# Optimization experiments

Measured on AMD Instinct MI355X. Metric: run time of the kernel, lower is better.

The kernel has to match this reference:

```python
import jax, jax.numpy as jnp
import numpy as np

N = 8192        # nodes in batch
E = 262144      # edges (avg degree 32)
IN_C = 64
OUT_C = 64
K = 3           # max_k
G = 64          # graphs in batch
NC = 10         # n_class
EPS = 1e-5      # batchnorm eps


def setup_inputs() -> dict:
    key = jax.random.key(0)
    ks = jax.random.split(key, 16)
    D_in = IN_C * K    # 192
    D_out = OUT_C * K  # 192
    inp = {
        'x': jax.random.normal(ks[0], (N, IN_C), jnp.float32),
        'edge_index': jax.random.randint(ks[1], (2, E), 0, N, dtype=jnp.int64),
        'batch': jnp.sort(jax.random.randint(ks[2], (N,), 0, G, dtype=jnp.int64)),
        # spectral-normed masked linear
        'W_orig': jax.random.normal(ks[3], (D_out, D_in), jnp.float32) * 0.05,
        'b': jnp.zeros((D_out,), jnp.float32),
        'u': jax.random.normal(ks[4], (D_out,), jnp.float32),
        # batchnorms (training-mode batch stats)
        'bn1_gamma': jnp.ones((D_out,), jnp.float32),
        'bn1_beta': jnp.zeros((D_out,), jnp.float32),
        'bn2_gamma': jnp.ones((D_out * 3,), jnp.float32),
        'bn2_beta': jnp.zeros((D_out * 3,), jnp.float32),
        # funnel head
        'w1': jax.random.normal(ks[5], (D_out * 2, D_out * 3), jnp.float32) * 0.05,
        'b1': jnp.zeros((D_out * 2,), jnp.float32),
        'w2': jax.random.normal(ks[6], (D_out, D_out * 2), jnp.float32) * 0.05,
        'b2': jnp.zeros((D_out,), jnp.float32),
        'w3': jax.random.normal(ks[7], (NC, D_out), jnp.float32) * 0.05,
        'b3': jnp.zeros((NC,), jnp.float32),
    }
    return inp


def _forward(x, edge_index, batch, W_orig, b, u, bn1_gamma, bn1_beta,
             bn2_gamma, bn2_beta, w1, b1, w2, b2, w3, b3):
    n = x.shape[0]
    row, col = edge_index[0], edge_index[1]
    # sym-normalized Laplacian L = I - D^-1/2 A D^-1/2, densified ([N,N])
    deg = jnp.zeros((n,), x.dtype).at[row].add(1.0)
    dinv = jnp.where(deg > 0, jax.lax.rsqrt(jnp.maximum(deg, 1.0)), 0.0)
    vals = -dinv[row] * dinv[col]
    L = jnp.zeros((n, n), x.dtype).at[row, col].add(vals)
    idx = jnp.arange(n)
    L = L.at[idx, idx].add(1.0)
    Hs = [x]
    h = x
    for _ in range(K - 1):
        h = L @ h
        Hs.append(h)
    Hcat = jnp.concatenate(Hs, axis=1)              # [N, IN_C*K]
    # spectral norm of W (one power-iteration step with stored u)
    v = W_orig.T @ u
    v = v / (jnp.linalg.norm(v) + 1e-12)
    sigma = u @ (W_orig @ v)
    W = W_orig / sigma
    # block lower-triangular mask: block i passes first IN_C*(i+1) input cols
    col_idx = jnp.arange(IN_C * K)
    row_block = jnp.arange(OUT_C * K) // OUT_C
    mask = (col_idx[None, :] < IN_C * (row_block[:, None] + 1)).astype(W.dtype)
    H = Hcat @ (W * mask).T + b                     # masked linear
    # reservoir_act_fun is identity (default)
    mu, var = H.mean(0), H.var(0)                   # BN (batch stats)
    H = bn1_gamma * (H - mu) * jax.lax.rsqrt(var + EPS) + bn1_beta
    # fused-style triple pooling over graph ids
    Hsum = jax.ops.segment_sum(H, batch, num_segments=G)
    cnt = jax.ops.segment_sum(jnp.ones((n,), H.dtype), batch, num_segments=G)
    Havg = Hsum / jnp.maximum(cnt, 1.0)[:, None]
    Hmax = jax.ops.segment_max(H, batch, num_segments=G)
    Hg = jnp.concatenate([Havg, Hsum, Hmax], axis=1)  # [G, 3*OUT_C*K]
    mu2, var2 = Hg.mean(0), Hg.var(0)
    xo = bn2_gamma * (Hg - mu2) * jax.lax.rsqrt(var2 + EPS) + bn2_beta
    # funnel output (dropout = identity in eval)
    xo = jax.nn.relu(xo @ w1.T + b1)
    xo = jax.nn.relu(xo @ w2.T + b2)
    return jax.nn.log_softmax(xo @ w3.T + b3, axis=1)


def reference(x, edge_index, batch, W_orig, b, u, bn1_gamma, bn1_beta,
              bn2_gamma, bn2_beta, w1, b1, w2, b2, w3, b3):
    return _forward(x, edge_index, batch, W_orig, b, u, bn1_gamma, bn1_beta,
                    bn2_gamma, bn2_beta, w1, b1, w2, b2, w3, b3)
```

## Files before the change

### kernel.cpp

```cpp
#include <hip/hip_runtime.h>
#include <math.h>

#define NN   8192
#define EE   262144
#define CIN  64
#define DD   192
#define GG   64
#define NCLS 10
#define D3   576
#define F1   384
#define F2   192
#define EPSB 1e-5f
#define NB   64
#define EPB  (EE / NB)
#define PS   8

__global__ __launch_bounds__(1024) void count_kernel(const int* __restrict__ ei,
                                                     int* __restrict__ pcnt) {
    __shared__ int hist[NN];
    int b = blockIdx.x, t = threadIdx.x;
    int4* hz = (int4*)hist;
    for (int i = t; i < NN / 4; i += 1024) hz[i] = make_int4(0, 0, 0, 0);
    __syncthreads();
    int e0 = b * EPB;
    for (int i = t; i < EPB; i += 1024) atomicAdd(&hist[ei[e0 + i]], 1);
    __syncthreads();
    const int4* hs = (const int4*)hist;
    int4* p4 = (int4*)&pcnt[b * NN];
    for (int i = t; i < NN / 4; i += 1024) p4[i] = hs[i];
}

__global__ __launch_bounds__(256) void offs_kernel(int* __restrict__ pcnt,
                                                   int* __restrict__ deg,
                                                   float* __restrict__ dinv) {
    int i = blockIdx.x * 256 + threadIdx.x;
    int run = 0;
#pragma unroll
    for (int b = 0; b < NB; b++) {
        int v = pcnt[b * NN + i];
        pcnt[b * NN + i] = run;
        run += v;
    }
    deg[i] = run;
    dinv[i] = (run > 0) ? rsqrtf((float)run) : 0.f;
}

__global__ void scan_kernel(const int* __restrict__ deg, int* __restrict__ rowptr,
                            const int* __restrict__ batch, int* __restrict__ gstart) {
    __shared__ int part[256];
    int t = threadIdx.x;
    int local[32];
    int base = t * 32;
    int s = 0;
    for (int i = 0; i < 32; i++) { local[i] = s; s += deg[base + i]; }
    part[t] = s;
    __syncthreads();
    for (int off = 1; off < 256; off <<= 1) {
        int v = (t >= off) ? part[t - off] : 0;
        __syncthreads();
        part[t] += v;
        __syncthreads();
    }
    int prefix = (t > 0) ? part[t - 1] : 0;
    for (int i = 0; i < 32; i++) rowptr[base + i] = prefix + local[i];
    if (t == 255) rowptr[NN] = part[255];
    for (int i = t; i < NN; i += 256) {
        int b0 = batch[i];
        int b1 = (i + 1 < NN) ? batch[i + 1] : GG;
        if (i == 0) { for (int g = 0; g <= b0; g++) gstart[g] = 0; }
        for (int g = b0 + 1; g <= b1; g++) gstart[g] = i + 1;
    }
}

__global__ __launch_bounds__(1024) void scatter_kernel(const int* __restrict__ ei,
                                                       const int* __restrict__ rowptr,
                                                       const int* __restrict__ off,
                                                       unsigned short* __restrict__ csr_col) {
    __shared__ int cur[NN];
    int b = blockIdx.x, t = threadIdx.x;
    const int* ob = &off[b * NN];
    for (int i = t; i < NN; i += 1024) cur[i] = rowptr[i] + ob[i];
    __syncthreads();
    int e0 = b * EPB;
    for (int i = t; i < EPB; i += 1024) {
        int r = ei[e0 + i];
        int c = ei[EE + e0 + i];
        int pos = atomicAdd(&cur[r], 1);
        csr_col[pos] = (unsigned short)c;
    }
}

__global__ __launch_bounds__(256) void spmm_kernel(const float* __restrict__ hin,
    int in_stride, int in_off,
    const int* __restrict__ rowptr, const unsigned short* __restrict__ col,
    const float* __restrict__ dinv,
    float* __restrict__ Hcat, int coff, int write_self) {
    int idx = blockIdx.x * 256 + threadIdx.x;
    int row = idx >> 6;
    int lane = idx & 63;
    int s = rowptr[row], e = rowptr[row + 1];
    float acc0 = 0.f, acc1 = 0.f;
    int p = s;
    for (; p + 1 < e; p += 2) {
        int c0 = col[p], c1 = col[p + 1];
        acc0 += dinv[c0] * hin[c0 * in_stride + in_off + lane];
        acc1 += dinv[c1] * hin[c1 * in_stride + in_off + lane];
    }
    if (p < e) {
        int c = col[p];
        acc0 += dinv[c] * hin[c * in_stride + in_off + lane];
    }
    float acc = acc0 + acc1;
    float self = hin[row * in_stride + in_off + lane];
    Hcat[row * DD + coff + lane] = self - dinv[row] * acc;
    if (write_self) Hcat[row * DD + lane] = self;
}

__global__ __launch_bounds__(1024) void sigma_kernel(const float* __restrict__ W,
                                                     const float* __restrict__ u,
                                                     float* __restrict__ sig) {
    __shared__ float vp[768];
    __shared__ float vsh[DD];
    __shared__ float red[1024];
    int t = threadIdx.x;
    if (t < 768) {
        int c = t >> 2, j = t & 3;
        float s = 0.f;
        const float* Wc = W + c;
        for (int i = j * 48; i < j * 48 + 48; i++) s += Wc[i * DD] * u[i];
        vp[t] = s;
    }
    __syncthreads();
    float vv = 0.f;
    if (t < DD) {
        float v = vp[4 * t] + vp[4 * t + 1] + vp[4 * t + 2] + vp[4 * t + 3];
        vsh[t] = v;
        vv = v * v;
    }
    red[t] = vv;
    __syncthreads();
    for (int off = 512; off > 0; off >>= 1) {
        if (t < off) red[t] += red[t + off];
        __syncthreads();
    }
    float norm = sqrtf(red[0]) + 1e-12f;
    __syncthreads();
    float a = 0.f;
    for (int idx = t; idx < DD * DD; idx += 1024) {
        int r = idx / DD, c = idx - r * DD;
        a += u[r] * W[idx] * vsh[c];
    }
    red[t] = a;
    __syncthreads();
    for (int off = 512; off > 0; off >>= 1) {
        if (t < off) red[t] += red[t + off];
        __syncthreads();
    }
    if (t == 0) sig[0] = norm / red[0];
}

__global__ __launch_bounds__(256) void pack_kernel(const float* __restrict__ W,
    const float* __restrict__ w1, const float* __restrict__ w2,
    float* __restrict__ Wp, float* __restrict__ Wp1, float* __restrict__ Wp2) {
    int idx = blockIdx.x * 256 + threadIdx.x;
    if (idx < DD * DD) {
        int r = idx / DD, c = idx - r * DD;
        float m = (c < CIN * ((r >> 6) + 1)) ? 1.f : 0.f;
        Wp[((c >> 2) * DD + r) * 4 + (c & 3)] = m * W[idx];
    }
    int i1 = idx - DD * DD;
    if (i1 >= 0 && i1 < F1 * D3) {
        int t = i1 / D3, k = i1 - t * D3;
        Wp1[((k >> 2) * F1 + t) * 4 + (k & 3)] = w1[i1];
    }
    int i2 = idx - DD * DD - F1 * D3;
    if (i2 >= 0 && i2 < F2 * F1) {
        int t = i2 / F1, k = i2 - t * F1;
        Wp2[((k >> 2) * F2 + t) * 4 + (k & 3)] = w2[i2];
    }
}

__global__ __launch_bounds__(192) void gemm_kernel(float* __restrict__ Hcat,
    const float* __restrict__ Wp, const float* __restrict__ bias,
    const float* __restrict__ sig) {
    __shared__ float hs[16 * DD];
    int t = threadIdx.x;
    int n0 = blockIdx.x * 16;
    const float4* src = (const float4*)&Hcat[n0 * DD];
    float4* dst = (float4*)hs;
#pragma unroll
    for (int i = 0; i < 4; i++) dst[t + 192 * i] = src[t + 192 * i];
    __syncthreads();
    float acc[16];
#pragma unroll
    for (int r = 0; r < 16; r++) acc[r] = 0.f;
    const float4* Wp4 = (const float4*)Wp;
    for (int k4 = 0; k4 < DD / 4; k4++) {
        float4 w = Wp4[k4 * DD + t];
#pragma unroll
        for (int r = 0; r < 16; r++) {
            const float4 h = *(const float4*)&hs[r * DD + k4 * 4];
            acc[r] += h.x * w.x + h.y * w.y + h.z * w.z + h.w * w.w;
        }
    }
    float inv_sigma = sig[0];
    float bv = bias[t];
#pragma unroll
    for (int r = 0; r < 16; r++) Hcat[(n0 + r) * DD + t] = inv_sigma * acc[r] + bv;
}

__global__ __launch_bounds__(192) void pool_kernel(const float* __restrict__ H,
    const int* __restrict__ gstart,
    float* __restrict__ Psum, float* __restrict__ Psq,
    float* __restrict__ Pmin, float* __restrict__ Pmax) {
    int b = blockIdx.x;
    int g = b >> 3, s = b & 7, c = threadIdx.x;
    int beg = gstart[g], end = gstart[g + 1];
    float sum = 0.f, sq = 0.f, mn = INFINITY, mx = -INFINITY;
    for (int i = beg + s; i < end; i += PS) {
        float x = H[i * DD + c];
        sum += x; sq += x * x;
        mn = fminf(mn, x); mx = fmaxf(mx, x);
    }
    Psum[b * DD + c] = sum; Psq[b * DD + c] = sq;
    Pmin[b * DD + c] = mn;  Pmax[b * DD + c] = mx;
}

__global__ __launch_bounds__(64) void hg_kernel(
    const float* __restrict__ Psum, const float* __restrict__ Psq,
    const float* __restrict__ Pmin, const float* __restrict__ Pmax,
    const int* __restrict__ gstart,
    const float* __restrict__ g1, const float* __restrict__ be1,
    const float* __restrict__ g2, const float* __restrict__ be2,
    float* __restrict__ Hg) {
    int t = blockIdx.x;
    int g = threadIdx.x;
    int f = t / DD, c = t - f * DD;
    float Sg = 0.f, Qg = 0.f;
#pragma unroll
    for (int s = 0; s < PS; s++) {
        Sg += Psum[(g * PS + s) * DD + c];
        Qg += Psq[(g * PS + s) * DD + c];
    }
    float S = Sg, Q = Qg;
    for (int off = 32; off > 0; off >>= 1) {
        S += __shfl_xor(S, off);
        Q += __shfl_xor(Q, off);
    }
    float mu = S * (1.f / (float)NN);
    float var = Q * (1.f / (float)NN) - mu * mu;
    float sc = g1[c] * rsqrtf(var + EPSB);
    float bb = be1[c];
    float v;
    if (f == 2) {
        float mx = -INFINITY, mn = INFINITY;
#pragma unroll
        for (int s = 0; s < PS; s++) {
            mx = fmaxf(mx, Pmax[(g * PS + s) * DD + c]);
            mn = fminf(mn, Pmin[(g * PS + s) * DD + c]);
        }
        float raw = (sc >= 0.f) ? mx : mn;
        v = sc * (raw - mu) + bb;
    } else {
        float nf = (float)(gstart[g + 1] - gstart[g]);
        float hsum = sc * (Sg - nf * mu) + nf * bb;
        v = (f == 0) ? hsum / fmaxf(nf, 1.f) : hsum;
    }
    float s2 = v, ss2 = v * v;
    for (int off = 32; off > 0; off >>= 1) {
        s2 += __shfl_xor(s2, off);
        ss2 += __shfl_xor(ss2, off);
    }
    float m2 = s2 * (1.f / (float)GG);
    float var2 = ss2 * (1.f / (float)GG) - m2 * m2;
    float sc2 = g2[t] * rsqrtf(var2 + EPSB);
    Hg[g * D3 + t] = sc2 * (v - m2) + be2[t];
}

__global__ __launch_bounds__(F1) void funnel_kernel(const float* __restrict__ Hg,
    const float* __restrict__ Wp1, const float* __restrict__ b1,
    const float* __restrict__ Wp2, const float* __restrict__ b2,
    const float* __restrict__ w3, const float* __restrict__ b3,
    float* __restrict__ out) {
    __shared__ float hg[D3];
    __shared__ float x1[F1];
    __shared__ float x2[F2];
    __shared__ float lg[NCLS];
    __shared__ float s_lse;
    int g = blockIdx.x, t = threadIdx.x;
    for (int i = t; i < D3; i += F1) hg[i] = Hg[g * D3 + i];
    __syncthreads();
    {
        float a = b1[t];
        const float4* W4 = (const float4*)Wp1;
        for (int k4 = 0; k4 < D3 / 4; k4++) {
            float4 w = W4[k4 * F1 + t];
            const float4 h = *(const float4*)&hg[k4 * 4];
            a += w.x * h.x + w.y * h.y + w.z * h.z + w.w * h.w;
        }
        x1[t] = fmaxf(a, 0.f);
    }
    __syncthreads();
    if (t < F2) {
        float a = b2[t];
        const float4* W4 = (const float4*)Wp2;
        for (int k4 = 0; k4 < F1 / 4; k4++) {
            float4 w = W4[k4 * F2 + t];
            const float4 h = *(const float4*)&x1[k4 * 4];
            a += w.x * h.x + w.y * h.y + w.z * h.z + w.w * h.w;
        }
        x2[t] = fmaxf(a, 0.f);
    }
    __syncthreads();
    if (t < NCLS) {
        float a = b3[t];
        const float4* wr = (const float4*)&w3[t * F2];
        const float4* h4 = (const float4*)x2;
        for (int k = 0; k < F2 / 4; k++) {
            float4 w = wr[k], h = h4[k];
            a += w.x * h.x + w.y * h.y + w.z * h.z + w.w * h.w;
        }
        lg[t] = a;
    }
    __syncthreads();
    if (t == 0) {
        float m = lg[0];
        for (int i = 1; i < NCLS; i++) m = fmaxf(m, lg[i]);
        float se = 0.f;
        for (int i = 0; i < NCLS; i++) se += expf(lg[i] - m);
        s_lse = m + logf(se);
    }
    __syncthreads();
    if (t < NCLS) out[g * NCLS + t] = lg[t] - s_lse;
}


extern "C" void kernel_launch(void* const* d_in, const int* in_sizes, int n_in,
                              void* d_out, int out_size, void* d_ws, size_t ws_size,
                              hipStream_t stream) {
    (void)in_sizes; (void)n_in; (void)out_size; (void)ws_size;
    const float* x     = (const float*)d_in[0];
    const int*   ei    = (const int*)d_in[1];
    const int*   batch = (const int*)d_in[2];
    const float* W     = (const float*)d_in[3];
    const float* b     = (const float*)d_in[4];
    const float* u     = (const float*)d_in[5];
    const float* g1    = (const float*)d_in[6];
    const float* be1   = (const float*)d_in[7];
    const float* g2    = (const float*)d_in[8];
    const float* be2   = (const float*)d_in[9];
    const float* w1    = (const float*)d_in[10];
    const float* b1    = (const float*)d_in[11];
    const float* w2    = (const float*)d_in[12];
    const float* b2    = (const float*)d_in[13];
    const float* w3    = (const float*)d_in[14];
    const float* b3    = (const float*)d_in[15];
    float* out = (float*)d_out;
    char*  ws  = (char*)d_ws;

    int*            gstart  = (int*)(ws + 0);
    int*            rowptr  = (int*)(ws + 512);
    int*            deg     = (int*)(ws + 33536);
    float*          dinv    = (float*)(ws + 66304);
    float*          sig     = (float*)(ws + 99072);
    float*          Wp      = (float*)(ws + 99328);
    float*          Psum    = (float*)(ws + 246784);
    float*          Psq     = (float*)(ws + 640000);
    float*          Pmin    = (float*)(ws + 1033216);
    float*          Pmax    = (float*)(ws + 1426432);
    float*          Hg      = (float*)(ws + 1819648);
    unsigned short* csr_col = (unsigned short*)(ws + 1967104);
    float*          Wp1     = (float*)(ws + 2491392);
    float*          Wp2     = (float*)(ws + 3376128);
    int*            pcnt    = (int*)(ws + 3671040);
    float*          Hcat    = (float*)(ws + 5768192);

    sigma_kernel<<<1, 1024, 0, stream>>>(W, u, sig);
    pack_kernel<<<(DD * DD + F1 * D3 + F2 * F1) / 256, 256, 0, stream>>>(
        W, w1, w2, Wp, Wp1, Wp2);
    count_kernel<<<NB, 1024, 0, stream>>>(ei, pcnt);
    offs_kernel<<<NN / 256, 256, 0, stream>>>(pcnt, deg, dinv);
    scan_kernel<<<1, 256, 0, stream>>>(deg, rowptr, batch, gstart);
    scatter_kernel<<<NB, 1024, 0, stream>>>(ei, rowptr, pcnt, csr_col);
    spmm_kernel<<<NN * 64 / 256, 256, 0, stream>>>(x, CIN, 0, rowptr, csr_col, dinv, Hcat, CIN, 1);
    spmm_kernel<<<NN * 64 / 256, 256, 0, stream>>>(Hcat, DD, CIN, rowptr, csr_col, dinv, Hcat, 2 * CIN, 0);
    gemm_kernel<<<NN / 16, 192, 0, stream>>>(Hcat, Wp, b, sig);
    pool_kernel<<<GG * PS, 192, 0, stream>>>(Hcat, gstart, Psum, Psq, Pmin, Pmax);
    hg_kernel<<<D3, 64, 0, stream>>>(Psum, Psq, Pmin, Pmax, gstart, g1, be1, g2, be2, Hg);
    funnel_kernel<<<GG, F1, 0, stream>>>(Hg, Wp1, b1, Wp2, b2, w3, b3, out);
}
```

Before: 220.0 us.

## Merge sigma/pack and offs/scan kernels, unroll SpMM gather by four

Combines the spectral-norm sigma computation and the weight packing into one launch, with the last block doing sigma. Merges the per-node offset kernel and the single-block scan into one cooperative kernel that uses a grid sync. Widens the SpMM neighbor loop to four independent accumulators for more memory-level parallelism. Together these cut two launches from the chain, at the cost of cooperative-launch overhead and 1024-thread pack blocks.

```diff
diff --git a/kernel.cpp b/kernel.cpp
--- a/kernel.cpp
+++ b/kernel.cpp
@@ -1,5 +1,8 @@
 #include <hip/hip_runtime.h>
+#include <hip/hip_cooperative_groups.h>
 #include <math.h>
+
+namespace cg = cooperative_groups;
 
 #define NN   8192
 #define EE   262144
@@ -14,6 +17,68 @@
 #define NB   64
 #define EPB  (EE / NB)
 #define PS   8
+#define PACKN (DD * DD + F1 * D3 + F2 * F1)
+
+__global__ __launch_bounds__(1024) void prep_kernel(const float* __restrict__ W,
+    const float* __restrict__ u, const float* __restrict__ w1,
+    const float* __restrict__ w2, float* __restrict__ sig,
+    float* __restrict__ Wp, float* __restrict__ Wp1, float* __restrict__ Wp2) {
+    int b = blockIdx.x, t = threadIdx.x;
+    if (b < 324) {
+        int idx = b * 1024 + t;
+        if (idx < DD * DD) {
+            int r = idx / DD, c = idx - r * DD;
+            float m = (c < CIN * ((r >> 6) + 1)) ? 1.f : 0.f;
+            Wp[((c >> 2) * DD + r) * 4 + (c & 3)] = m * W[idx];
+        } else if (idx < DD * DD + F1 * D3) {
+            int i1 = idx - DD * DD;
+            int tt = i1 / D3, k = i1 - tt * D3;
+            Wp1[((k >> 2) * F1 + tt) * 4 + (k & 3)] = w1[i1];
+        } else {
+            int i2 = idx - DD * DD - F1 * D3;
+            int tt = i2 / F1, k = i2 - tt * F1;
+            Wp2[((k >> 2) * F2 + tt) * 4 + (k & 3)] = w2[i2];
+        }
+        return;
+    }
+    __shared__ float vp[768];
+    __shared__ float vsh[DD];
+    __shared__ float red[1024];
+    if (t < 768) {
+        int c = t >> 2, j = t & 3;
+        float s = 0.f;
+        const float* Wc = W + c;
+        for (int i = j * 48; i < j * 48 + 48; i++) s += Wc[i * DD] * u[i];
+        vp[t] = s;
+    }
+    __syncthreads();
+    float vv = 0.f;
+    if (t < DD) {
+        float v = vp[4 * t] + vp[4 * t + 1] + vp[4 * t + 2] + vp[4 * t + 3];
+        vsh[t] = v;
+        vv = v * v;
+    }
+    red[t] = vv;
+    __syncthreads();
+    for (int off = 512; off > 0; off >>= 1) {
+        if (t < off) red[t] += red[t + off];
+        __syncthreads();
+    }
+    float norm = sqrtf(red[0]) + 1e-12f;
+    __syncthreads();
+    float a = 0.f;
+    for (int idx = t; idx < DD * DD; idx += 1024) {
+        int r = idx / DD, c = idx - r * DD;
+        a += u[r] * W[idx] * vsh[c];
+    }
+    red[t] = a;
+    __syncthreads();
+    for (int off = 512; off > 0; off >>= 1) {
+        if (t < off) red[t] += red[t + off];
+        __syncthreads();
+    }
+    if (t == 0) sig[0] = norm / red[0];
+}
 
 __global__ __launch_bounds__(1024) void count_kernel(const int* __restrict__ ei,
                                                      int* __restrict__ pcnt) {
@@ -30,25 +95,27 @@
     for (int i = t; i < NN / 4; i += 1024) p4[i] = hs[i];
 }
 
-__global__ __launch_bounds__(256) void offs_kernel(int* __restrict__ pcnt,
-                                                   int* __restrict__ deg,
-                                                   float* __restrict__ dinv) {
-    int i = blockIdx.x * 256 + threadIdx.x;
-    int run = 0;
-#pragma unroll
-    for (int b = 0; b < NB; b++) {
-        int v = pcnt[b * NN + i];
-        pcnt[b * NN + i] = run;
-        run += v;
-    }
-    deg[i] = run;
-    dinv[i] = (run > 0) ? rsqrtf((float)run) : 0.f;
-}
-
-__global__ void scan_kernel(const int* __restrict__ deg, int* __restrict__ rowptr,
-                            const int* __restrict__ batch, int* __restrict__ gstart) {
+__global__ __launch_bounds__(256) void offs_scan_kernel(int* __restrict__ pcnt,
+    int* __restrict__ deg, float* __restrict__ dinv,
+    const int* __restrict__ batch, int* __restrict__ rowptr,
+    int* __restrict__ gstart) {
+    cg::grid_group grid = cg::this_grid();
+    int t = threadIdx.x;
+    {
+        int i = blockIdx.x * 256 + t;
+        int run = 0;
+#pragma unroll
+        for (int b = 0; b < NB; b++) {
+            int v = pcnt[b * NN + i];
+            pcnt[b * NN + i] = run;
+            run += v;
+        }
+        deg[i] = run;
+        dinv[i] = (run > 0) ? rsqrtf((float)run) : 0.f;
+    }
+    grid.sync();
+    if (blockIdx.x != 0) return;
     __shared__ int part[256];
-    int t = threadIdx.x;
     int local[32];
     int base = t * 32;
     int s = 0;
@@ -99,85 +166,23 @@
     int row = idx >> 6;
     int lane = idx & 63;
     int s = rowptr[row], e = rowptr[row + 1];
-    float acc0 = 0.f, acc1 = 0.f;
+    float a0 = 0.f, a1 = 0.f, a2 = 0.f, a3 = 0.f;
     int p = s;
-    for (; p + 1 < e; p += 2) {
-        int c0 = col[p], c1 = col[p + 1];
-        acc0 += dinv[c0] * hin[c0 * in_stride + in_off + lane];
-        acc1 += dinv[c1] * hin[c1 * in_stride + in_off + lane];
-    }
-    if (p < e) {
+    for (; p + 3 < e; p += 4) {
+        int c0 = col[p], c1 = col[p + 1], c2 = col[p + 2], c3 = col[p + 3];
+        a0 += dinv[c0] * hin[c0 * in_stride + in_off + lane];
+        a1 += dinv[c1] * hin[c1 * in_stride + in_off + lane];
+        a2 += dinv[c2] * hin[c2 * in_stride + in_off + lane];
+        a3 += dinv[c3] * hin[c3 * in_stride + in_off + lane];
+    }
+    for (; p < e; p++) {
         int c = col[p];
-        acc0 += dinv[c] * hin[c * in_stride + in_off + lane];
-    }
-    float acc = acc0 + acc1;
+        a0 += dinv[c] * hin[c * in_stride + in_off + lane];
+    }
+    float acc = (a0 + a1) + (a2 + a3);
     float self = hin[row * in_stride + in_off + lane];
     Hcat[row * DD + coff + lane] = self - dinv[row] * acc;
     if (write_self) Hcat[row * DD + lane] = self;
-}
-
-__global__ __launch_bounds__(1024) void sigma_kernel(const float* __restrict__ W,
-                                                     const float* __restrict__ u,
-                                                     float* __restrict__ sig) {
-    __shared__ float vp[768];
-    __shared__ float vsh[DD];
-    __shared__ float red[1024];
-    int t = threadIdx.x;
-    if (t < 768) {
-        int c = t >> 2, j = t & 3;
-        float s = 0.f;
-        const float* Wc = W + c;
-        for (int i = j * 48; i < j * 48 + 48; i++) s += Wc[i * DD] * u[i];
-        vp[t] = s;
-    }
-    __syncthreads();
-    float vv = 0.f;
-    if (t < DD) {
-        float v = vp[4 * t] + vp[4 * t + 1] + vp[4 * t + 2] + vp[4 * t + 3];
-        vsh[t] = v;
-        vv = v * v;
-    }
-    red[t] = vv;
-    __syncthreads();
-    for (int off = 512; off > 0; off >>= 1) {
-        if (t < off) red[t] += red[t + off];
-        __syncthreads();
-    }
-    float norm = sqrtf(red[0]) + 1e-12f;
-    __syncthreads();
-    float a = 0.f;
-    for (int idx = t; idx < DD * DD; idx += 1024) {
-        int r = idx / DD, c = idx - r * DD;
-        a += u[r] * W[idx] * vsh[c];
-    }
-    red[t] = a;
-    __syncthreads();
-    for (int off = 512; off > 0; off >>= 1) {
-        if (t < off) red[t] += red[t + off];
-        __syncthreads();
-    }
-    if (t == 0) sig[0] = norm / red[0];
-}
-
-__global__ __launch_bounds__(256) void pack_kernel(const float* __restrict__ W,
-    const float* __restrict__ w1, const float* __restrict__ w2,
-    float* __restrict__ Wp, float* __restrict__ Wp1, float* __restrict__ Wp2) {
-    int idx = blockIdx.x * 256 + threadIdx.x;
-    if (idx < DD * DD) {
-        int r = idx / DD, c = idx - r * DD;
-        float m = (c < CIN * ((r >> 6) + 1)) ? 1.f : 0.f;
-        Wp[((c >> 2) * DD + r) * 4 + (c & 3)] = m * W[idx];
-    }
-    int i1 = idx - DD * DD;
-    if (i1 >= 0 && i1 < F1 * D3) {
-        int t = i1 / D3, k = i1 - t * D3;
-        Wp1[((k >> 2) * F1 + t) * 4 + (k & 3)] = w1[i1];
-    }
-    int i2 = idx - DD * DD - F1 * D3;
-    if (i2 >= 0 && i2 < F2 * F1) {
-        int t = i2 / F1, k = i2 - t * F1;
-        Wp2[((k >> 2) * F2 + t) * 4 + (k & 3)] = w2[i2];
-    }
 }
 
 __global__ __launch_bounds__(192) void gemm_kernel(float* __restrict__ Hcat,
@@ -375,12 +380,14 @@
     int*            pcnt    = (int*)(ws + 3671040);
     float*          Hcat    = (float*)(ws + 5768192);
 
-    sigma_kernel<<<1, 1024, 0, stream>>>(W, u, sig);
-    pack_kernel<<<(DD * DD + F1 * D3 + F2 * F1) / 256, 256, 0, stream>>>(
-        W, w1, w2, Wp, Wp1, Wp2);
+    prep_kernel<<<325, 1024, 0, stream>>>(W, u, w1, w2, sig, Wp, Wp1, Wp2);
     count_kernel<<<NB, 1024, 0, stream>>>(ei, pcnt);
-    offs_kernel<<<NN / 256, 256, 0, stream>>>(pcnt, deg, dinv);
-    scan_kernel<<<1, 256, 0, stream>>>(deg, rowptr, batch, gstart);
+    {
+        void* args[] = { (void*)&pcnt, (void*)&deg, (void*)&dinv,
+                         (void*)&batch, (void*)&rowptr, (void*)&gstart };
+        hipLaunchCooperativeKernel((void*)offs_scan_kernel, dim3(32), dim3(256),
+                                   args, 0, stream);
+    }
     scatter_kernel<<<NB, 1024, 0, stream>>>(ei, rowptr, pcnt, csr_col);
     spmm_kernel<<<NN * 64 / 256, 256, 0, stream>>>(x, CIN, 0, rowptr, csr_col, dinv, Hcat, CIN, 1);
     spmm_kernel<<<NN * 64 / 256, 256, 0, stream>>>(Hcat, DD, CIN, rowptr, csr_col, dinv, Hcat, 2 * CIN, 0);
```

Result: slower. 253.9 us (+15.4%).
